# Kernel tuning notes

Hardware: AMD Instinct MI355X
Metric: run time of the kernel (lower is better)

## Reference

```python
import jax, jax.numpy as jnp
import numpy as np

HEADS = 16

def setup_inputs() -> dict:
    key = jax.random.key(0)
    ks = jax.random.split(key, 12)
    S, E = 2048, 1024
    x = jax.random.normal(ks[0], (S, E), dtype=jnp.float32)
    seg = jnp.sort(jax.random.randint(ks[1], (S,), 0, 32)).astype(jnp.int32)
    sc = 1.0 / np.sqrt(E)
    Wq = jax.random.normal(ks[2], (E, E), dtype=jnp.float32) * sc
    bq = jax.random.normal(ks[3], (E,), dtype=jnp.float32) * 0.01
    Wk = jax.random.normal(ks[4], (E, E), dtype=jnp.float32) * sc
    bk = jax.random.normal(ks[5], (E,), dtype=jnp.float32) * 0.01
    Wv = jax.random.normal(ks[6], (E, E), dtype=jnp.float32) * sc
    bv = jax.random.normal(ks[7], (E,), dtype=jnp.float32) * 0.01
    Wo = jax.random.normal(ks[8], (E, E), dtype=jnp.float32) * sc
    bo = jax.random.normal(ks[9], (E,), dtype=jnp.float32) * 0.01
    return {"x": x, "seg": seg, "pos": 1000,
            "Wq": Wq, "bq": bq, "Wk": Wk, "bk": bk,
            "Wv": Wv, "bv": bv, "Wo": Wo, "bo": bo}

def reference(x, seg, pos, Wq, bq, Wk, bk, Wv, bv, Wo, bo):
    S, E = x.shape
    H = HEADS
    d = E // H
    # projections: [S,E] -> [H,S,d]
    q = (x @ Wq + bq).reshape(S, H, d).transpose(1, 0, 2)
    k = (x @ Wk + bk).reshape(S, H, d).transpose(1, 0, 2)
    v = (x @ Wv + bv).reshape(S, H, d).transpose(1, 0, 2)
    # raw scores (note: original code applies NO 1/sqrt(d) scaling)
    scores = jnp.einsum('hid,hjd->hij', q, k)  # [H,S,S]
    same_seg = seg[:, None] == seg[None, :]    # [S,S]
    # faithful to original: out-of-segment entries stay ZERO (not -inf)
    scores = jnp.where(same_seg[None, :, :], scores, 0.0)
    weights = jax.nn.softmax(scores, axis=-1)
    out = jnp.einsum('hij,hjd->hid', weights, v)          # [H,S,d]
    out = out.transpose(1, 0, 2).reshape(S, E)            # [S,E]
    result = out @ Wo + bo                                # [S,E]
    # mean over the segment containing `pos`
    m = (seg == seg[pos]).astype(result.dtype)            # [S]
    return (result * m[:, None]).sum(axis=0) / m.sum()
```

## Files before the change

### kernel.cpp

```cpp
#include <hip/hip_runtime.h>

#define SS 2048
#define EE 1024
#define NH 16
#define DH 64
#define NR 128


__device__ __forceinline__ int rfl(int v) {
    return __builtin_amdgcn_readfirstlane(v);
}

__device__ __forceinline__ int2 seg_bounds(const int* __restrict__ seg,
                                           const int* __restrict__ pos) {
    __shared__ int sb[32];
    int t = threadIdx.x, nthr = blockDim.x;
    int g = seg[pos[0]];
    int lomin = SS, himax = 0;
    const int4* s4 = (const int4*)seg;
    for (int i = t; i < SS / 4; i += nthr) {
        int4 v = s4[i];
        int b = i * 4;
        if (v.x == g) { lomin = min(lomin, b);     himax = max(himax, b + 1); }
        if (v.y == g) { lomin = min(lomin, b + 1); himax = max(himax, b + 2); }
        if (v.z == g) { lomin = min(lomin, b + 2); himax = max(himax, b + 3); }
        if (v.w == g) { lomin = min(lomin, b + 3); himax = max(himax, b + 4); }
    }
    for (int o = 32; o; o >>= 1) {
        lomin = min(lomin, __shfl_xor(lomin, o, 64));
        himax = max(himax, __shfl_xor(himax, o, 64));
    }
    if ((t & 63) == 0) { sb[t >> 6] = lomin; sb[16 + (t >> 6)] = himax; }
    __syncthreads();
    int nw = nthr >> 6;
    lomin = SS; himax = 0;
    for (int wq = 0; wq < nw; ++wq) {
        lomin = min(lomin, sb[wq]);
        himax = max(himax, sb[16 + wq]);
    }
    return make_int2(lomin, himax);
}

__global__ void __launch_bounds__(1024, 4) k_d1(
    const float* __restrict__ x, const int* __restrict__ seg,
    const int* __restrict__ pos,
    const float* __restrict__ Wq, const float* __restrict__ bq,
    const float* __restrict__ Wk, const float* __restrict__ bk,
    const float* __restrict__ Wv, const float* __restrict__ bv,
    float* __restrict__ xpart, int* __restrict__ meta,
    float* __restrict__ A, float* __restrict__ Bh,
    float* __restrict__ Q, float* __restrict__ K, float* __restrict__ V,
    int nmax) {
    __shared__ float red[4096];
    const int t = threadIdx.x, wv = t >> 6, lane = t & 63;

    if (blockIdx.z == 0) {
        if (blockIdx.y == 0) {
            int xb = blockIdx.x;
            int col4 = t & 255, rgrp = t >> 8;
            const float4* x4 = (const float4*)x
                + (size_t)(xb * 128 + rgrp * 32) * 256 + col4;
            float4 a = make_float4(0.f, 0.f, 0.f, 0.f);
#pragma unroll 8
            for (int r = 0; r < 32; ++r) {
                float4 v = x4[(size_t)r * 256];
                a.x += v.x; a.y += v.y; a.z += v.z; a.w += v.w;
            }
            ((float4*)(xpart + (size_t)(xb * 4 + rgrp) * EE))[col4] = a;
        } else if (blockIdx.y == 1 && blockIdx.x == 0) {
            A[t] = 0.f;
            if (t < 16) Bh[t] = 0.f;
            int2 bnd = seg_bounds(seg, pos);
            if (t == 0) { meta[0] = bnd.x; meta[1] = bnd.y; }
        }
        return;
    }

    int2 bnd = seg_bounds(seg, pos);
    int lo = bnd.x;
    int nc = bnd.y - lo; if (nc > nmax) nc = nmax; if (nc < 1) nc = 1;
    int mat = blockIdx.z - 1;
    const float* W  = mat == 0 ? Wq : mat == 1 ? Wk : Wv;
    const float* bb = mat == 0 ? bq : mat == 1 ? bk : bv;
    float* dst      = mat == 0 ? Q  : mat == 1 ? K  : V;
    int e = blockIdx.x * 64 + lane;
    int kbu = rfl(wv) * 64;
    const float* Wp = W + (size_t)kbu * EE + e;

    for (int rt = blockIdx.y; rt * 4 < nc; rt += 16) {
        int r0 = rt * 4;
        int rB = min(r0 + 1, nc - 1);
        int rC = min(r0 + 2, nc - 1);
        int rD = min(r0 + 3, nc - 1);
        const float* xA = x + (size_t)rfl(lo + r0) * EE + kbu;
        const float* xB = x + (size_t)rfl(lo + rB) * EE + kbu;
        const float* xC = x + (size_t)rfl(lo + rC) * EE + kbu;
        const float* xD = x + (size_t)rfl(lo + rD) * EE + kbu;
        float a0 = 0.f, a1 = 0.f, a2 = 0.f, a3 = 0.f;
#pragma unroll 8
        for (int c = 0; c < 64; ++c) {
            float wj = Wp[(size_t)c * EE];
            a0 += xA[c] * wj;
            a1 += xB[c] * wj;
            a2 += xC[c] * wj;
            a3 += xD[c] * wj;
        }
        __syncthreads();
        red[((wv << 2) + 0) * 64 + lane] = a0;
        red[((wv << 2) + 1) * 64 + lane] = a1;
        red[((wv << 2) + 2) * 64 + lane] = a2;
        red[((wv << 2) + 3) * 64 + lane] = a3;
        __syncthreads();
        if (t < 256) {
            int row = t >> 6, col = t & 63;
            float s = 0.f;
#pragma unroll
            for (int w = 0; w < 16; ++w)
                s += red[((w << 2) + row) * 64 + col];
            s += bb[blockIdx.x * 64 + col];
            int gr = r0 + row;
            if (gr < nc)
                dst[(size_t)gr * EE + blockIdx.x * 64 + col] = s;
        }
    }
}

__global__ void __launch_bounds__(256, 4) k_d2(
    const float* __restrict__ Wv, const float* __restrict__ bv,
    const float* __restrict__ xpart, const int* __restrict__ meta,
    const float* __restrict__ Q, const float* __restrict__ K,
    const float* __restrict__ V,
    float* __restrict__ vtot, float* __restrict__ A, float* __restrict__ Bh,
    int nmax) {
    __shared__ float lds[2048];
    const int t = threadIdx.x, wv = t >> 6, lane = t & 63;
    const int bid = blockIdx.x, gb = gridDim.x;

    if (bid < 16) {
        float4 a = make_float4(0.f, 0.f, 0.f, 0.f);
        const float4* xp4 = (const float4*)xpart + t;
#pragma unroll 8
        for (int b = 0; b < 64; ++b) {
            float4 v = xp4[(size_t)b * 256];
            a.x += v.x; a.y += v.y; a.z += v.z; a.w += v.w;
        }
        ((float4*)lds)[t] = a;
        __syncthreads();
        int e = bid * 64 + lane;
        int kbu = rfl(wv) * 256;
        const float* Wp = Wv + (size_t)kbu * EE + e;
        const float4* xs4 = (const float4*)(lds + kbu);
        float acc = 0.f;
#pragma unroll 4
        for (int c = 0; c < 256; c += 4) {
            float4 xv = xs4[c >> 2];
            acc += xv.x * Wp[(size_t)(c + 0) * EE]
                 + xv.y * Wp[(size_t)(c + 1) * EE]
                 + xv.z * Wp[(size_t)(c + 2) * EE]
                 + xv.w * Wp[(size_t)(c + 3) * EE];
        }
        __syncthreads();
        lds[1024 + wv * 64 + lane] = acc;
        __syncthreads();
        if (wv == 0) {
            float s = lds[1024 + lane] + lds[1088 + lane]
                    + lds[1152 + lane] + lds[1216 + lane];
            vtot[e] = s + bv[e] * (float)SS;
        }
        return;
    }

    int lo = meta[0];
    int nc = meta[1] - lo; if (nc > nmax) nc = nmax; if (nc < 1) nc = 1;
    int nit = nc * NH;
    float* ql = lds + wv * 512;
    float* sb = ql + 64;
    for (int it = (bid - 16) * 4 + wv; it < nit; it += (gb - 16) * 4) {
        int r = it >> 4, h = it & 15;
        ql[lane] = Q[(size_t)r * EE + h * DH + lane];
        asm volatile("s_waitcnt lgkmcnt(0)" ::: "memory");
        const float4* q4 = (const float4*)ql;
        float m = 0.f;
        for (int j = lane; j < nc; j += 64) {
            const float4* kr = (const float4*)(K + (size_t)j * EE + h * DH);
            float s = 0.f;
#pragma unroll 4
            for (int d = 0; d < DH / 4; ++d) {
                float4 kv = kr[d];
                float4 qv = q4[d];
                s += qv.x * kv.x + qv.y * kv.y + qv.z * kv.z + qv.w * kv.w;
            }
            sb[j] = s;
            m = fmaxf(m, s);
        }
        for (int o = 32; o; o >>= 1) m = fmaxf(m, __shfl_xor(m, o, 64));
        float dl = 0.f;
        for (int j = lane; j < nc; j += 64) {
            float wgt = __expf(sb[j] - m);
            sb[j] = wgt;
            dl += wgt;
        }
        for (int o = 32; o; o >>= 1) dl += __shfl_xor(dl, o, 64);
        float em = __expf(-m);
        float denom = dl + (float)(SS - nc) * em;
        asm volatile("s_waitcnt lgkmcnt(0)" ::: "memory");
        float acc = 0.f, vs = 0.f;
        const float* Vp = V + h * DH + lane;
        int j = 0;
        for (; j + 4 <= nc; j += 4) {
            float4 wq = *(const float4*)(sb + j);
            float v0 = Vp[(size_t)(j + 0) * EE];
            float v1 = Vp[(size_t)(j + 1) * EE];
            float v2 = Vp[(size_t)(j + 2) * EE];
            float v3 = Vp[(size_t)(j + 3) * EE];
            acc += wq.x * v0 + wq.y * v1 + wq.z * v2 + wq.w * v3;
            vs  += v0 + v1 + v2 + v3;
        }
        for (; j < nc; ++j) {
            float v0 = Vp[(size_t)j * EE];
            acc += sb[j] * v0;
            vs  += v0;
        }
        atomicAdd(&A[h * DH + lane], (acc - vs * em) / denom);
        if (lane == 0) atomicAdd(&Bh[h], em / denom);
    }
}

__global__ void __launch_bounds__(1024, 4) k_d3(
    const int* __restrict__ meta,
    const float* __restrict__ Wo, const float* __restrict__ bo,
    const float* __restrict__ vtot, const float* __restrict__ A,
    const float* __restrict__ Bh, int nmax, float* __restrict__ out) {
    __shared__ float lds[2048];
    const int t = threadIdx.x, wv = t >> 6, lane = t & 63;
    int nc = meta[1] - meta[0]; if (nc > nmax) nc = nmax; if (nc < 1) nc = 1;
    lds[t] = A[t] + vtot[t] * Bh[t >> 6];
    __syncthreads();
    int e = blockIdx.x * 64 + lane;
    int kbu = rfl(wv) * 64;
    const float* Wp = Wo + (size_t)kbu * EE + e;
    float a = 0.f;
#pragma unroll 8
    for (int c = 0; c < 64; ++c)
        a += lds[kbu + c] * Wp[(size_t)c * EE];
    lds[1024 + wv * 64 + lane] = a;
    __syncthreads();
    if (t < 64) {
        float s = 0.f;
#pragma unroll
        for (int w = 0; w < 16; ++w)
            s += lds[1024 + w * 64 + t];
        out[blockIdx.x * 64 + t] = bo[blockIdx.x * 64 + t] + s / (float)nc;
    }
}

extern "C" void kernel_launch(void* const* d_in, const int* in_sizes, int n_in,
                              void* d_out, int out_size, void* d_ws, size_t ws_size,
                              hipStream_t stream) {
    const float* x  = (const float*)d_in[0];
    const int* seg  = (const int*)d_in[1];
    const int* pos  = (const int*)d_in[2];
    const float* Wq = (const float*)d_in[3];
    const float* bq = (const float*)d_in[4];
    const float* Wk = (const float*)d_in[5];
    const float* bk = (const float*)d_in[6];
    const float* Wv = (const float*)d_in[7];
    const float* bv = (const float*)d_in[8];
    const float* Wo = (const float*)d_in[9];
    const float* bo = (const float*)d_in[10];
    float* out = (float*)d_out;

    char* w = (char*)d_ws;
    float* A     = (float*)(w + 0);
    float* Bh    = (float*)(w + 4096);
    int*   meta  = (int*)(w + 4160);
    float* vtot  = (float*)(w + 8192);
    float* xpart = (float*)(w + 16384);

    size_t base = 16384 + 64 * EE * sizeof(float);
    size_t avail = (ws_size > base) ? ws_size - base : 0;
    int nmax = (int)(avail / (3ull * EE * sizeof(float)));
    if (nmax > NR) nmax = NR;
    if (nmax < 1) nmax = 1;
    float* Q = (float*)(w + base);
    float* K = Q + (size_t)nmax * EE;
    float* V = K + (size_t)nmax * EE;

    k_d1<<<dim3(16, 16, 4), 1024, 0, stream>>>(
        x, seg, pos, Wq, bq, Wk, bk, Wv, bv, xpart, meta, A, Bh, Q, K, V, nmax);
    k_d2<<<272, 256, 0, stream>>>(
        Wv, bv, xpart, meta, Q, K, V, vtot, A, Bh, nmax);
    k_d3<<<16, 1024, 0, stream>>>(meta, Wo, bo, vtot, A, Bh, nmax, out);
}
```

Before: 137.8 us.

## Fuse output projection into attention kernel via grid-wide spin barrier

Removes the third kernel launch by having the first 16 blocks of k_d2 spin-wait on a global counter until all attention blocks finish, then compute the Wo projection and write the output. The column-sum of x is spread over 64 blocks instead of 16, with more partials to reduce in k_d2. The QKV projection now processes 8 rows per iteration instead of 4. The spin barrier assumes all 272 blocks are co-resident, which risks deadlock and adds polling latency.

```diff
diff --git a/kernel.cpp b/kernel.cpp
--- a/kernel.cpp
+++ b/kernel.cpp
@@ -51,27 +51,27 @@
     float* __restrict__ A, float* __restrict__ Bh,
     float* __restrict__ Q, float* __restrict__ K, float* __restrict__ V,
     int nmax) {
-    __shared__ float red[4096];
+    __shared__ float red[8192];
     const int t = threadIdx.x, wv = t >> 6, lane = t & 63;
 
     if (blockIdx.z == 0) {
-        if (blockIdx.y == 0) {
-            int xb = blockIdx.x;
+        if (blockIdx.y < 4) {
+            int xb = blockIdx.y * 16 + blockIdx.x;
             int col4 = t & 255, rgrp = t >> 8;
             const float4* x4 = (const float4*)x
-                + (size_t)(xb * 128 + rgrp * 32) * 256 + col4;
+                + (size_t)(xb * 32 + rgrp) * 256 + col4;
             float4 a = make_float4(0.f, 0.f, 0.f, 0.f);
 #pragma unroll 8
-            for (int r = 0; r < 32; ++r) {
-                float4 v = x4[(size_t)r * 256];
+            for (int r = 0; r < 8; ++r) {
+                float4 v = x4[(size_t)(r * 4) * 256];
                 a.x += v.x; a.y += v.y; a.z += v.z; a.w += v.w;
             }
             ((float4*)(xpart + (size_t)(xb * 4 + rgrp) * EE))[col4] = a;
-        } else if (blockIdx.y == 1 && blockIdx.x == 0) {
+        } else if (blockIdx.y == 4 && blockIdx.x == 0) {
             A[t] = 0.f;
             if (t < 16) Bh[t] = 0.f;
             int2 bnd = seg_bounds(seg, pos);
-            if (t == 0) { meta[0] = bnd.x; meta[1] = bnd.y; }
+            if (t == 0) { meta[0] = bnd.x; meta[1] = bnd.y; meta[2] = 0; }
         }
         return;
     }
@@ -87,16 +87,25 @@
     int kbu = rfl(wv) * 64;
     const float* Wp = W + (size_t)kbu * EE + e;
 
-    for (int rt = blockIdx.y; rt * 4 < nc; rt += 16) {
-        int r0 = rt * 4;
-        int rB = min(r0 + 1, nc - 1);
-        int rC = min(r0 + 2, nc - 1);
-        int rD = min(r0 + 3, nc - 1);
+    for (int rt = blockIdx.y; rt * 8 < nc; rt += 16) {
+        int r0 = rt * 8;
+        int r1 = min(r0 + 1, nc - 1);
+        int r2 = min(r0 + 2, nc - 1);
+        int r3 = min(r0 + 3, nc - 1);
+        int r4 = min(r0 + 4, nc - 1);
+        int r5 = min(r0 + 5, nc - 1);
+        int r6 = min(r0 + 6, nc - 1);
+        int r7 = min(r0 + 7, nc - 1);
         const float* xA = x + (size_t)rfl(lo + r0) * EE + kbu;
-        const float* xB = x + (size_t)rfl(lo + rB) * EE + kbu;
-        const float* xC = x + (size_t)rfl(lo + rC) * EE + kbu;
-        const float* xD = x + (size_t)rfl(lo + rD) * EE + kbu;
+        const float* xB = x + (size_t)rfl(lo + r1) * EE + kbu;
+        const float* xC = x + (size_t)rfl(lo + r2) * EE + kbu;
+        const float* xD = x + (size_t)rfl(lo + r3) * EE + kbu;
+        const float* xE = x + (size_t)rfl(lo + r4) * EE + kbu;
+        const float* xF = x + (size_t)rfl(lo + r5) * EE + kbu;
+        const float* xG = x + (size_t)rfl(lo + r6) * EE + kbu;
+        const float* xH = x + (size_t)rfl(lo + r7) * EE + kbu;
         float a0 = 0.f, a1 = 0.f, a2 = 0.f, a3 = 0.f;
+        float a4 = 0.f, a5 = 0.f, a6 = 0.f, a7 = 0.f;
 #pragma unroll 8
         for (int c = 0; c < 64; ++c) {
             float wj = Wp[(size_t)c * EE];
@@ -104,19 +113,28 @@
             a1 += xB[c] * wj;
             a2 += xC[c] * wj;
             a3 += xD[c] * wj;
-        }
-        __syncthreads();
-        red[((wv << 2) + 0) * 64 + lane] = a0;
-        red[((wv << 2) + 1) * 64 + lane] = a1;
-        red[((wv << 2) + 2) * 64 + lane] = a2;
-        red[((wv << 2) + 3) * 64 + lane] = a3;
-        __syncthreads();
-        if (t < 256) {
+            a4 += xE[c] * wj;
+            a5 += xF[c] * wj;
+            a6 += xG[c] * wj;
+            a7 += xH[c] * wj;
+        }
+        __syncthreads();
+        int rb = (wv << 3) * 64 + lane;
+        red[rb + 0 * 64] = a0;
+        red[rb + 1 * 64] = a1;
+        red[rb + 2 * 64] = a2;
+        red[rb + 3 * 64] = a3;
+        red[rb + 4 * 64] = a4;
+        red[rb + 5 * 64] = a5;
+        red[rb + 6 * 64] = a6;
+        red[rb + 7 * 64] = a7;
+        __syncthreads();
+        if (t < 512) {
             int row = t >> 6, col = t & 63;
             float s = 0.f;
 #pragma unroll
             for (int w = 0; w < 16; ++w)
-                s += red[((w << 2) + row) * 64 + col];
+                s += red[((w << 3) + row) * 64 + col];
             s += bb[blockIdx.x * 64 + col];
             int gr = r0 + row;
             if (gr < nc)
@@ -127,11 +145,12 @@
 
 __global__ void __launch_bounds__(256, 4) k_d2(
     const float* __restrict__ Wv, const float* __restrict__ bv,
-    const float* __restrict__ xpart, const int* __restrict__ meta,
+    const float* __restrict__ Wo, const float* __restrict__ bo,
+    const float* __restrict__ xpart, int* __restrict__ meta,
     const float* __restrict__ Q, const float* __restrict__ K,
     const float* __restrict__ V,
     float* __restrict__ vtot, float* __restrict__ A, float* __restrict__ Bh,
-    int nmax) {
+    int nmax, float* __restrict__ out) {
     __shared__ float lds[2048];
     const int t = threadIdx.x, wv = t >> 6, lane = t & 63;
     const int bid = blockIdx.x, gb = gridDim.x;
@@ -140,7 +159,7 @@
         float4 a = make_float4(0.f, 0.f, 0.f, 0.f);
         const float4* xp4 = (const float4*)xpart + t;
 #pragma unroll 8
-        for (int b = 0; b < 64; ++b) {
+        for (int b = 0; b < 256; ++b) {
             float4 v = xp4[(size_t)b * 256];
             a.x += v.x; a.y += v.y; a.z += v.z; a.w += v.w;
         }
@@ -165,7 +184,46 @@
         if (wv == 0) {
             float s = lds[1024 + lane] + lds[1088 + lane]
                     + lds[1152 + lane] + lds[1216 + lane];
-            vtot[e] = s + bv[e] * (float)SS;
+            atomicExch(&vtot[e], s + bv[e] * (float)SS);
+        }
+        if (t == 0) {
+            atomicAdd(&meta[2], 1);
+            while (atomicAdd(&meta[2], 0) < (int)gb)
+                __builtin_amdgcn_s_sleep(8);
+        }
+        __syncthreads();
+        if (t < 16) lds[1280 + t] = atomicAdd(&Bh[t], 0.f);
+        __syncthreads();
+        {
+            int c0 = t * 4;
+#pragma unroll
+            for (int i = 0; i < 4; ++i) {
+                int c = c0 + i;
+                float av = atomicAdd(&A[c], 0.f);
+                float vv = atomicAdd(&vtot[c], 0.f);
+                lds[c] = av + vv * lds[1280 + (c >> 6)];
+            }
+        }
+        __syncthreads();
+        int nc = meta[1] - meta[0]; if (nc > nmax) nc = nmax; if (nc < 1) nc = 1;
+        const float* Wp2 = Wo + (size_t)kbu * EE + e;
+        const float4* os4 = (const float4*)(lds + kbu);
+        float a3 = 0.f;
+#pragma unroll 4
+        for (int c = 0; c < 256; c += 4) {
+            float4 ov = os4[c >> 2];
+            a3 += ov.x * Wp2[(size_t)(c + 0) * EE]
+                + ov.y * Wp2[(size_t)(c + 1) * EE]
+                + ov.z * Wp2[(size_t)(c + 2) * EE]
+                + ov.w * Wp2[(size_t)(c + 3) * EE];
+        }
+        __syncthreads();
+        lds[1024 + wv * 64 + lane] = a3;
+        __syncthreads();
+        if (wv == 0) {
+            float s = lds[1024 + lane] + lds[1088 + lane]
+                    + lds[1152 + lane] + lds[1216 + lane];
+            out[e] = bo[e] + s / (float)nc;
         }
         return;
     }
@@ -224,34 +282,8 @@
         atomicAdd(&A[h * DH + lane], (acc - vs * em) / denom);
         if (lane == 0) atomicAdd(&Bh[h], em / denom);
     }
-}
-
-__global__ void __launch_bounds__(1024, 4) k_d3(
-    const int* __restrict__ meta,
-    const float* __restrict__ Wo, const float* __restrict__ bo,
-    const float* __restrict__ vtot, const float* __restrict__ A,
-    const float* __restrict__ Bh, int nmax, float* __restrict__ out) {
-    __shared__ float lds[2048];
-    const int t = threadIdx.x, wv = t >> 6, lane = t & 63;
-    int nc = meta[1] - meta[0]; if (nc > nmax) nc = nmax; if (nc < 1) nc = 1;
-    lds[t] = A[t] + vtot[t] * Bh[t >> 6];
     __syncthreads();
-    int e = blockIdx.x * 64 + lane;
-    int kbu = rfl(wv) * 64;
-    const float* Wp = Wo + (size_t)kbu * EE + e;
-    float a = 0.f;
-#pragma unroll 8
-    for (int c = 0; c < 64; ++c)
-        a += lds[kbu + c] * Wp[(size_t)c * EE];
-    lds[1024 + wv * 64 + lane] = a;
-    __syncthreads();
-    if (t < 64) {
-        float s = 0.f;
-#pragma unroll
-        for (int w = 0; w < 16; ++w)
-            s += lds[1024 + w * 64 + t];
-        out[blockIdx.x * 64 + t] = bo[blockIdx.x * 64 + t] + s / (float)nc;
-    }
+    if (t == 0) atomicAdd(&meta[2], 1);
 }
 
 extern "C" void kernel_launch(void* const* d_in, const int* in_sizes, int n_in,
@@ -277,7 +309,7 @@
     float* vtot  = (float*)(w + 8192);
     float* xpart = (float*)(w + 16384);
 
-    size_t base = 16384 + 64 * EE * sizeof(float);
+    size_t base = 16384 + 256ull * EE * sizeof(float);
     size_t avail = (ws_size > base) ? ws_size - base : 0;
     int nmax = (int)(avail / (3ull * EE * sizeof(float)));
     if (nmax > NR) nmax = NR;
@@ -289,6 +321,5 @@
     k_d1<<<dim3(16, 16, 4), 1024, 0, stream>>>(
         x, seg, pos, Wq, bq, Wk, bk, Wv, bv, xpart, meta, A, Bh, Q, K, V, nmax);
     k_d2<<<272, 256, 0, stream>>>(
-        Wv, bv, xpart, meta, Q, K, V, vtot, A, Bh, nmax);
-    k_d3<<<16, 1024, 0, stream>>>(meta, Wo, bo, vtot, A, Bh, nmax, out);
-}
+        Wv, bv, Wo, bo, xpart, meta, Q, K, V, vtot, A, Bh, nmax, out);
+}
```

Result: slower. 147.4 us (+7.0%).

## Split vtot GEMV across K-quarters with atomics and widen k_d1 row tiles to 8

Applied to the files above, without the earlier changes.

The column-sum times Wv product (vtot) moves from 16 blocks to 64 blocks, each covering a quarter of the reduction dimension, and the partials are combined with atomicAdd into a vtot buffer that k_d1 now zeroes. Separately, the QKV projection in k_d1 computes 8 rows per tile instead of 4, so each loaded weight value is reused across more rows, at the cost of a doubled LDS reduction buffer and more registers. The attention blocks in k_d2 shift their index offset to account for the extra vtot blocks, and the grid grows to 320.

```diff
diff --git a/kernel.cpp b/kernel.cpp
--- a/kernel.cpp
+++ b/kernel.cpp
@@ -48,10 +48,10 @@
     const float* __restrict__ Wk, const float* __restrict__ bk,
     const float* __restrict__ Wv, const float* __restrict__ bv,
     float* __restrict__ xpart, int* __restrict__ meta,
-    float* __restrict__ A, float* __restrict__ Bh,
+    float* __restrict__ A, float* __restrict__ Bh, float* __restrict__ vtot,
     float* __restrict__ Q, float* __restrict__ K, float* __restrict__ V,
     int nmax) {
-    __shared__ float red[4096];
+    __shared__ float red[8192];
     const int t = threadIdx.x, wv = t >> 6, lane = t & 63;
 
     if (blockIdx.z == 0) {
@@ -69,6 +69,7 @@
             ((float4*)(xpart + (size_t)(xb * 4 + rgrp) * EE))[col4] = a;
         } else if (blockIdx.y == 1 && blockIdx.x == 0) {
             A[t] = 0.f;
+            vtot[t] = 0.f;
             if (t < 16) Bh[t] = 0.f;
             int2 bnd = seg_bounds(seg, pos);
             if (t == 0) { meta[0] = bnd.x; meta[1] = bnd.y; }
@@ -87,16 +88,25 @@
     int kbu = rfl(wv) * 64;
     const float* Wp = W + (size_t)kbu * EE + e;
 
-    for (int rt = blockIdx.y; rt * 4 < nc; rt += 16) {
-        int r0 = rt * 4;
-        int rB = min(r0 + 1, nc - 1);
-        int rC = min(r0 + 2, nc - 1);
-        int rD = min(r0 + 3, nc - 1);
+    for (int rt = blockIdx.y; rt * 8 < nc; rt += 16) {
+        int r0 = rt * 8;
+        int r1 = min(r0 + 1, nc - 1);
+        int r2 = min(r0 + 2, nc - 1);
+        int r3 = min(r0 + 3, nc - 1);
+        int r4 = min(r0 + 4, nc - 1);
+        int r5 = min(r0 + 5, nc - 1);
+        int r6 = min(r0 + 6, nc - 1);
+        int r7 = min(r0 + 7, nc - 1);
         const float* xA = x + (size_t)rfl(lo + r0) * EE + kbu;
-        const float* xB = x + (size_t)rfl(lo + rB) * EE + kbu;
-        const float* xC = x + (size_t)rfl(lo + rC) * EE + kbu;
-        const float* xD = x + (size_t)rfl(lo + rD) * EE + kbu;
+        const float* xB = x + (size_t)rfl(lo + r1) * EE + kbu;
+        const float* xC = x + (size_t)rfl(lo + r2) * EE + kbu;
+        const float* xD = x + (size_t)rfl(lo + r3) * EE + kbu;
+        const float* xE = x + (size_t)rfl(lo + r4) * EE + kbu;
+        const float* xF = x + (size_t)rfl(lo + r5) * EE + kbu;
+        const float* xG = x + (size_t)rfl(lo + r6) * EE + kbu;
+        const float* xH = x + (size_t)rfl(lo + r7) * EE + kbu;
         float a0 = 0.f, a1 = 0.f, a2 = 0.f, a3 = 0.f;
+        float a4 = 0.f, a5 = 0.f, a6 = 0.f, a7 = 0.f;
 #pragma unroll 8
         for (int c = 0; c < 64; ++c) {
             float wj = Wp[(size_t)c * EE];
@@ -104,19 +114,28 @@
             a1 += xB[c] * wj;
             a2 += xC[c] * wj;
             a3 += xD[c] * wj;
+            a4 += xE[c] * wj;
+            a5 += xF[c] * wj;
+            a6 += xG[c] * wj;
+            a7 += xH[c] * wj;
         }
         __syncthreads();
-        red[((wv << 2) + 0) * 64 + lane] = a0;
-        red[((wv << 2) + 1) * 64 + lane] = a1;
-        red[((wv << 2) + 2) * 64 + lane] = a2;
-        red[((wv << 2) + 3) * 64 + lane] = a3;
+        int rb = (wv << 3) * 64 + lane;
+        red[rb + 0 * 64] = a0;
+        red[rb + 1 * 64] = a1;
+        red[rb + 2 * 64] = a2;
+        red[rb + 3 * 64] = a3;
+        red[rb + 4 * 64] = a4;
+        red[rb + 5 * 64] = a5;
+        red[rb + 6 * 64] = a6;
+        red[rb + 7 * 64] = a7;
         __syncthreads();
-        if (t < 256) {
+        if (t < 512) {
             int row = t >> 6, col = t & 63;
             float s = 0.f;
 #pragma unroll
             for (int w = 0; w < 16; ++w)
-                s += red[((w << 2) + row) * 64 + col];
+                s += red[((w << 3) + row) * 64 + col];
             s += bb[blockIdx.x * 64 + col];
             int gr = r0 + row;
             if (gr < nc)
@@ -136,37 +155,26 @@
     const int t = threadIdx.x, wv = t >> 6, lane = t & 63;
     const int bid = blockIdx.x, gb = gridDim.x;
 
-    if (bid < 16) {
-        float4 a = make_float4(0.f, 0.f, 0.f, 0.f);
-        const float4* xp4 = (const float4*)xpart + t;
-#pragma unroll 8
-        for (int b = 0; b < 64; ++b) {
-            float4 v = xp4[(size_t)b * 256];
-            a.x += v.x; a.y += v.y; a.z += v.z; a.w += v.w;
-        }
-        ((float4*)lds)[t] = a;
+    if (bid < 64) {
+        int ct = bid & 15;
+        int kq = bid >> 4;
+        float s = 0.f;
+        const float* xp = xpart + kq * 256 + t;
+#pragma unroll 8
+        for (int b = 0; b < 64; ++b)
+            s += xp[(size_t)b * EE];
+        lds[t] = s;
         __syncthreads();
-        int e = bid * 64 + lane;
-        int kbu = rfl(wv) * 256;
-        const float* Wp = Wv + (size_t)kbu * EE + e;
-        const float4* xs4 = (const float4*)(lds + kbu);
-        float acc = 0.f;
-#pragma unroll 4
-        for (int c = 0; c < 256; c += 4) {
-            float4 xv = xs4[c >> 2];
-            acc += xv.x * Wp[(size_t)(c + 0) * EE]
-                 + xv.y * Wp[(size_t)(c + 1) * EE]
-                 + xv.z * Wp[(size_t)(c + 2) * EE]
-                 + xv.w * Wp[(size_t)(c + 3) * EE];
-        }
-        __syncthreads();
-        lds[1024 + wv * 64 + lane] = acc;
-        __syncthreads();
-        if (wv == 0) {
-            float s = lds[1024 + lane] + lds[1088 + lane]
-                    + lds[1152 + lane] + lds[1216 + lane];
-            vtot[e] = s + bv[e] * (float)SS;
-        }
+        int e = ct * 64 + lane;
+        int kwu = rfl(wv) * 64;
+        const float* Wp = Wv + (size_t)(kq * 256 + kwu) * EE + e;
+        const float* xq = lds + kwu;
+        float a = 0.f;
+#pragma unroll 8
+        for (int c = 0; c < 64; ++c)
+            a += xq[c] * Wp[(size_t)c * EE];
+        if (kq == 0 && wv == 0) a += bv[e] * (float)SS;
+        atomicAdd(&vtot[e], a);
         return;
     }
 
@@ -175,7 +183,7 @@
     int nit = nc * NH;
     float* ql = lds + wv * 512;
     float* sb = ql + 64;
-    for (int it = (bid - 16) * 4 + wv; it < nit; it += (gb - 16) * 4) {
+    for (int it = (bid - 64) * 4 + wv; it < nit; it += (gb - 64) * 4) {
         int r = it >> 4, h = it & 15;
         ql[lane] = Q[(size_t)r * EE + h * DH + lane];
         asm volatile("s_waitcnt lgkmcnt(0)" ::: "memory");
@@ -277,7 +285,7 @@
     float* vtot  = (float*)(w + 8192);
     float* xpart = (float*)(w + 16384);
 
-    size_t base = 16384 + 64 * EE * sizeof(float);
+    size_t base = 16384 + 64ull * EE * sizeof(float);
     size_t avail = (ws_size > base) ? ws_size - base : 0;
     int nmax = (int)(avail / (3ull * EE * sizeof(float)));
     if (nmax > NR) nmax = NR;
@@ -287,8 +295,9 @@
     float* V = K + (size_t)nmax * EE;
 
     k_d1<<<dim3(16, 16, 4), 1024, 0, stream>>>(
-        x, seg, pos, Wq, bq, Wk, bk, Wv, bv, xpart, meta, A, Bh, Q, K, V, nmax);
-    k_d2<<<272, 256, 0, stream>>>(
+        x, seg, pos, Wq, bq, Wk, bk, Wv, bv, xpart, meta, A, Bh, vtot,
+        Q, K, V, nmax);
+    k_d2<<<320, 256, 0, stream>>>(
         Wv, bv, xpart, meta, Q, K, V, vtot, A, Bh, nmax);
     k_d3<<<16, 1024, 0, stream>>>(meta, Wo, bo, vtot, A, Bh, nmax, out);
 }
```

Result: no change. 138.8 us (median of 2 runs) (+0.8%).
